# Kernel tuning notes

Hardware: AMD Instinct MI355X
Metric: run time of the kernel (lower is better)

## Reference

```python
import jax, jax.numpy as jnp
import numpy as np

TEMPERATURE = 0.1
EPS = 1e-12  # tf.math.l2_normalize epsilon

BATCH = 512
DIM = 256
QUEUE = 65536


def l2_normalize(x, axis=1):
    sq = jnp.sum(x * x, axis=axis, keepdims=True)
    return x * jax.lax.rsqrt(jnp.maximum(sq, EPS))


def setup_inputs() -> dict:
    key = jax.random.key(0)
    k1, k2, k3 = jax.random.split(key, 3)
    projections_1 = jax.random.normal(k1, (BATCH, DIM), dtype=jnp.float32)
    projections_2 = jax.random.normal(k2, (BATCH, DIM), dtype=jnp.float32)
    feature_queue = l2_normalize(jax.random.normal(k3, (QUEUE, DIM), dtype=jnp.float32), axis=1)
    return {"projections_1": projections_1, "projections_2": projections_2, "feature_queue": feature_queue}


def nearest_neighbour(projections, feature_queue):
    # [B, Q] similarity vs the memory queue, 1-NN retrieval + gather
    support_similarities = jnp.einsum('bd,qd->bq', projections, feature_queue)
    nn_idx = jnp.argmax(support_similarities, axis=1)
    nn_projections = feature_queue[nn_idx]  # [B, D]
    # straight-through: forward value is nn, gradient flows to projections
    return projections + jax.lax.stop_gradient(nn_projections - projections)


def reference(projections_1, projections_2, feature_queue):
    p1 = l2_normalize(projections_1, axis=1)
    p2 = l2_normalize(projections_2, axis=1)

    nn1 = nearest_neighbour(p1, feature_queue)
    nn2 = nearest_neighbour(p2, feature_queue)

    s_1_2_1 = jnp.einsum('bd,cd->bc', nn1, p2) / TEMPERATURE
    s_1_2_2 = jnp.einsum('bd,cd->bc', p2, nn1) / TEMPERATURE
    s_2_1_1 = jnp.einsum('bd,cd->bc', nn2, p1) / TEMPERATURE
    s_2_1_2 = jnp.einsum('bd,cd->bc', p1, nn2) / TEMPERATURE

    logits = jnp.concatenate([s_1_2_1, s_1_2_2, s_2_1_1, s_2_1_2], axis=0)  # [4B, B]
    batch = p1.shape[0]
    labels = jnp.tile(jnp.arange(batch), 4)  # [4B]

    # sparse categorical crossentropy from logits
    logp = jax.nn.log_softmax(logits, axis=-1)
    loss = -logp[jnp.arange(4 * batch), labels]  # [4B]

    # FIFO queue update (normalized projections_1 pushed in front)
    new_queue = jnp.concatenate([p1, feature_queue[:-batch]], axis=0)
    return loss, new_queue
```

## Files before the change

kernel.cpp:

```cpp
#include <hip/hip_runtime.h>
#include <stdint.h>


#define BATCH  512
#define DIM    256
#define QUEUE  65536
#define MROWS  1024
#define NGRP   2048
#define MARGIN 0.01f

typedef short bf16x8 __attribute__((ext_vector_type(8)));
typedef float f32x4  __attribute__((ext_vector_type(4)));

__device__ __forceinline__ unsigned int mono_f32(float f) {
    unsigned int u = __float_as_uint(f);
    return (u & 0x80000000u) ? ~u : (u | 0x80000000u);
}
__device__ __forceinline__ float unmono_f32(unsigned int m) {
    unsigned int u = (m & 0x80000000u) ? (m ^ 0x80000000u) : ~m;
    return __uint_as_float(u);
}
__device__ __forceinline__ unsigned short f2bf(float f) {
    unsigned int u = __float_as_uint(f);
    return (unsigned short)((u + 0x7fffu + ((u >> 16) & 1u)) >> 16);
}

__global__ void k1_norm(const float* __restrict__ p1, const float* __restrict__ p2,
                        float* __restrict__ Pn, float* __restrict__ PnT,
                        unsigned short* __restrict__ PhiF, float* __restrict__ outq,
                        int* __restrict__ npairs, unsigned int* __restrict__ rowmaxU,
                        unsigned long long* __restrict__ rowfinal)
{
    const int r = blockIdx.x;
    const int t = threadIdx.x;
    if (t == 0) {
        rowmaxU[r] = 0u;
        rowfinal[r] = 0ull;
        if (r == 0) *npairs = 0;
    }
    const float* src = (r < BATCH) ? p1 : p2;
    const int row = (r < BATCH) ? r : r - BATCH;
    float4 v = ((const float4*)(src + (size_t)row * DIM))[t];
    float sq = v.x*v.x + v.y*v.y + v.z*v.z + v.w*v.w;
    #pragma unroll
    for (int off = 32; off; off >>= 1) sq += __shfl_xor(sq, off, 64);
    sq = fmaxf(sq, 1e-12f);
    float s = rsqrtf(sq);
    s = s * (1.5f - 0.5f * sq * s * s);
    v.x *= s; v.y *= s; v.z *= s; v.w *= s;
    ((float4*)(Pn + (size_t)r * DIM))[t] = v;
    const int k = t * 4;
    PnT[(size_t)(k + 0) * MROWS + r] = v.x;
    PnT[(size_t)(k + 1) * MROWS + r] = v.y;
    PnT[(size_t)(k + 2) * MROWS + r] = v.z;
    PnT[(size_t)(k + 3) * MROWS + r] = v.w;
    short4 b;
    b.x = (short)f2bf(v.x); b.y = (short)f2bf(v.y);
    b.z = (short)f2bf(v.z); b.w = (short)f2bf(v.w);
    {
        const int c = t >> 1;
        const int idx = ((r >> 4) * 8 + (c >> 2)) * 64 + (c & 3) * 16 + (r & 15);
        *(short4*)((char*)PhiF + (size_t)idx * 16 + (t & 1) * 8) = b;
    }
    if (r < BATCH) ((float4*)(outq + (size_t)r * DIM))[t] = v;
}

__global__ void k0_prep(const float* __restrict__ queue, float* __restrict__ outq,
                        char* __restrict__ Qbf)
{
    const int b = blockIdx.x;
    const int t = threadIdx.x;
    const int n0 = b * 64;
    const f32x4* qsrc = (const f32x4*)(queue + (size_t)n0 * DIM);
    f32x4* qdst = (f32x4*)(outq + (size_t)(n0 + BATCH) * DIM);
    char* tile = Qbf + (size_t)b * 32768;
    #pragma unroll 4
    for (int it = 0; it < 16; ++it) {
        const int L = it * 256 + t;
        const int r = L >> 6, h = L & 63;
        f32x4 v = qsrc[(size_t)r * 64 + h];
        if (n0 + r < QUEUE - BATCH)
            __builtin_nontemporal_store(v, qdst + (size_t)r * 64 + h);
        short4 bb;
        bb.x = (short)f2bf(v.x); bb.y = (short)f2bf(v.y);
        bb.z = (short)f2bf(v.z); bb.w = (short)f2bf(v.w);
        const int c16 = h >> 1, hf = h & 1;
        *(short4*)(tile + r * 512 + ((c16 ^ (r & 31)) << 4) + hf * 8) = bb;
    }
}

__device__ __forceinline__ void k2_stage_async(const char* __restrict__ tile,
                                               char* Bsb, int t)
{
    #pragma unroll
    for (int it = 0; it < 8; ++it) {
        const int L = it * 256 + t;
        __builtin_amdgcn_global_load_lds(
            (const __attribute__((address_space(1))) unsigned int*)(tile + (size_t)L * 16),
            (__attribute__((address_space(3))) unsigned int*)(Bsb + L * 16), 16, 0, 0);
    }
}

__global__ __launch_bounds__(256, 2)
void k2_mfma(const unsigned short* __restrict__ PhiF, const char* __restrict__ Qbf,
             float* __restrict__ cand)
{
    __shared__ __align__(16) char Bs[2][32768];
    const int bid = blockIdx.x;
    const int s = bid >> 8;
    const int c = bid & 255;
    const int t  = threadIdx.x;
    const int w  = t >> 6, lane = t & 63;
    const int lr = lane & 15, q = lane >> 4;
    const int mbase = s * 256 + w * 64;
    const char* chunkbase = Qbf + (size_t)(c * 4) * 32768;

    bf16x8 pfr[4][8];
    {
        const char* Pw = (const char*)PhiF;
        const int mt16b = mbase >> 4;
        #pragma unroll
        for (int mj = 0; mj < 4; ++mj)
            #pragma unroll
            for (int ks = 0; ks < 8; ++ks)
                pfr[mj][ks] = *(const bf16x8*)(Pw + ((size_t)((mt16b + mj) * 8 + ks) * 64 + lane) * 16);
    }

    k2_stage_async(chunkbase, Bs[0], t);
    __syncthreads();

    for (int tl = 0; tl < 4; ++tl) {
        if (tl < 3)
            k2_stage_async(chunkbase + (size_t)(tl + 1) * 32768, Bs[(tl + 1) & 1], t);

        char* Bsb = Bs[tl & 1];
        f32x4 acc[4][4];
        #pragma unroll
        for (int i = 0; i < 4; ++i)
            #pragma unroll
            for (int j = 0; j < 4; ++j) acc[i][j] = (f32x4){0.f, 0.f, 0.f, 0.f};

        #pragma unroll
        for (int ks = 0; ks < 8; ++ks) {
            bf16x8 qf[4];
            #pragma unroll
            for (int ni = 0; ni < 4; ++ni) {
                const int r = ni * 16 + lr;
                const int c16 = ks * 4 + q;
                qf[ni] = *(const bf16x8*)(Bsb + r * 512 + ((c16 ^ (r & 31)) << 4));
            }
            #pragma unroll
            for (int ni = 0; ni < 4; ++ni)
                #pragma unroll
                for (int mj = 0; mj < 4; ++mj)
                    acc[ni][mj] = __builtin_amdgcn_mfma_f32_16x16x32_bf16(qf[ni], pfr[mj][ks], acc[ni][mj], 0, 0, 0);
        }

        #pragma unroll
        for (int mj = 0; mj < 4; ++mj) {
            #pragma unroll
            for (int gl = 0; gl < 2; ++gl) {
                f32x4 va = acc[2 * gl][mj], vb = acc[2 * gl + 1][mj];
                float mx = fmaxf(fmaxf(fmaxf(va[0], va[1]), fmaxf(va[2], va[3])),
                                 fmaxf(fmaxf(vb[0], vb[1]), fmaxf(vb[2], vb[3])));
                mx = fmaxf(mx, __shfl_xor(mx, 16, 64));
                mx = fmaxf(mx, __shfl_xor(mx, 32, 64));
                if (q == 0)
                    cand[(size_t)(c * 8 + tl * 2 + gl) * MROWS + (mbase + mj * 16 + lr)] = mx;
            }
        }
        __syncthreads();
    }
}

__global__ void k2b_rowmax(const float* __restrict__ cand, unsigned int* __restrict__ rowmaxU)
{
    const int t  = threadIdx.x;
    const int ml = t & 63, gs = t >> 6;
    const int mc = blockIdx.x & 15, gc = blockIdx.x >> 4;
    const int m  = mc * 64 + ml;
    const int g0 = gc * 128 + gs * 32;
    float mx = -1e30f;
    #pragma unroll 8
    for (int j = 0; j < 32; ++j)
        mx = fmaxf(mx, cand[(size_t)(g0 + j) * MROWS + m]);
    __shared__ float pm[4][64];
    pm[gs][ml] = mx;
    __syncthreads();
    if (gs == 0) {
        mx = fmaxf(fmaxf(pm[0][ml], pm[1][ml]), fmaxf(pm[2][ml], pm[3][ml]));
        atomicMax(rowmaxU + m, mono_f32(mx));
    }
}

__global__ void k2c_filter(const float* __restrict__ cand, const unsigned int* __restrict__ rowmaxU,
                           unsigned int* __restrict__ pairs, int* __restrict__ npairs)
{
    const int t  = threadIdx.x;
    const int ml = t & 63, gs = t >> 6;
    const int mc = blockIdx.x & 15, gc = blockIdx.x >> 4;
    const int m  = mc * 64 + ml;
    const int g0 = gc * 128 + gs * 32;
    const float thr = unmono_f32(rowmaxU[m]) - MARGIN;
    #pragma unroll 8
    for (int j = 0; j < 32; ++j) {
        if (cand[(size_t)(g0 + j) * MROWS + m] >= thr) {
            int p = atomicAdd(npairs, 1);
            pairs[p] = ((unsigned int)m << 16) | (unsigned int)(g0 + j);
        }
    }
}

__global__ __launch_bounds__(256, 4)
void k2d_rescore(const unsigned int* __restrict__ pairs, const int* __restrict__ npairs,
                 const float* __restrict__ Pn, const float* __restrict__ queue,
                 unsigned long long* __restrict__ rowfinal)
{
    const int t = threadIdx.x, w = t >> 6, lane = t & 63;
    const int n = *npairs;
    const int col_l = lane & 31, half = lane >> 5;
    for (int p = blockIdx.x * 4 + w; p < n; p += gridDim.x * 4) {
        const unsigned int pr = pairs[p];
        const int row = pr >> 16, g = pr & 0xffff;
        const int col = g * 32 + col_l;
        const float4* qp = (const float4*)(queue + (size_t)col * DIM + half * 128);
        const float4* pp = (const float4*)(Pn + (size_t)row * DIM + half * 128);
        float4 sv = {0.f, 0.f, 0.f, 0.f};
        #pragma unroll 8
        for (int j = 0; j < 32; ++j) {
            float4 a = pp[j], b = qp[j];
            sv.x = fmaf(a.x, b.x, sv.x); sv.y = fmaf(a.y, b.y, sv.y);
            sv.z = fmaf(a.z, b.z, sv.z); sv.w = fmaf(a.w, b.w, sv.w);
        }
        float s = (sv.x + sv.y) + (sv.z + sv.w);
        s += __shfl_xor(s, 32, 64);
        unsigned long long best = ((unsigned long long)mono_f32(s) << 32)
                                | (unsigned int)(65535 - col);
        #pragma unroll
        for (int off = 1; off <= 16; off <<= 1) {
            unsigned long long o = __shfl_xor(best, off, 64);
            best = best > o ? best : o;
        }
        if (lane == 0) atomicMax(rowfinal + row, best);
    }
}

__global__ void k3_sim(const unsigned long long* __restrict__ rowfinal,
                       const float* __restrict__ queue,
                       const float* __restrict__ PnT, float* __restrict__ S)
{
    const int b  = blockIdx.x;
    const int rb = (b >> 1) * 8;
    const int ch = b & 1;
    const int tid = threadIdx.x;
    const int which = (rb < BATCH) ? 0 : 1;
    const int colbase = which ? 0 : BATCH;
    const int col = colbase + ch * 256 + tid;
    __shared__ float nnv[8][DIM];
    #pragma unroll
    for (int j = 0; j < 8; ++j) {
        const int idx = 65535 - (int)(rowfinal[rb + j] & 0xFFFFull);
        nnv[j][tid] = queue[(size_t)idx * DIM + tid];
    }
    __syncthreads();
    float acc[8];
    #pragma unroll
    for (int j = 0; j < 8; ++j) acc[j] = 0.f;
    for (int k4 = 0; k4 < 64; ++k4) {
        float4 nv[8];
        #pragma unroll
        for (int j = 0; j < 8; ++j) nv[j] = ((const float4*)nnv[j])[k4];
        #pragma unroll
        for (int kk = 0; kk < 4; ++kk) {
            const int k = k4 * 4 + kk;
            const float v0 = PnT[(size_t)k * MROWS + col];
            #pragma unroll
            for (int j = 0; j < 8; ++j) {
                const float nj = ((const float*)&nv[j])[kk];
                acc[j] = fmaf(nj, v0, acc[j]);
            }
        }
    }
    const int i0 = rb & (BATCH - 1);
    float* Sout = S + (size_t)which * (BATCH * BATCH);
    #pragma unroll
    for (int j = 0; j < 8; ++j)
        Sout[(size_t)(i0 + j) * BATCH + ch * 256 + tid] = acc[j] * 10.0f;
}

__global__ void k4_loss(const float* __restrict__ S, float* __restrict__ loss)
{
    const int r = blockIdx.x;
    const int tid = threadIdx.x;
    const int grp = r >> 9;
    const int i = r & 511;
    const float* M = S + (size_t)(grp >> 1) * (BATCH * BATCH);
    float x0, x1;
    if (!(grp & 1)) { x0 = M[(size_t)i * BATCH + tid];  x1 = M[(size_t)i * BATCH + tid + 256]; }
    else            { x0 = M[(size_t)tid * BATCH + i];  x1 = M[(size_t)(tid + 256) * BATCH + i]; }
    const float diag = M[(size_t)i * BATCH + i];
    float mx = fmaxf(x0, x1);
    #pragma unroll
    for (int off = 1; off < 64; off <<= 1) mx = fmaxf(mx, __shfl_xor(mx, off, 64));
    __shared__ float redm[4], reds[4];
    if ((tid & 63) == 0) redm[tid >> 6] = mx;
    __syncthreads();
    mx = fmaxf(fmaxf(redm[0], redm[1]), fmaxf(redm[2], redm[3]));
    float e = __expf(x0 - mx) + __expf(x1 - mx);
    #pragma unroll
    for (int off = 1; off < 64; off <<= 1) e += __shfl_xor(e, off, 64);
    if ((tid & 63) == 0) reds[tid >> 6] = e;
    __syncthreads();
    if (tid == 0)
        loss[r] = mx + logf(reds[0] + reds[1] + reds[2] + reds[3]) - diag;
}

extern "C" void kernel_launch(void* const* d_in, const int* in_sizes, int n_in,
                              void* d_out, int out_size, void* d_ws, size_t ws_size,
                              hipStream_t stream)
{
    const float* p1    = (const float*)d_in[0];
    const float* p2    = (const float*)d_in[1];
    const float* queue = (const float*)d_in[2];
    float* out  = (float*)d_out;
    float* loss = out;
    float* outq = out + 4 * BATCH;

    char* w = (char*)d_ws;
    float* cand = (float*)w;                               w += (size_t)NGRP * MROWS * 4;
    unsigned long long* rowfinal = (unsigned long long*)w; w += MROWS * 8;
    unsigned int* rowmaxU = (unsigned int*)w;              w += MROWS * 4;
    float* Pn  = (float*)w;                                w += (size_t)MROWS * DIM * 4;
    float* PnT = (float*)w;                                w += (size_t)MROWS * DIM * 4;
    unsigned short* PhiF = (unsigned short*)w;             w += (size_t)MROWS * DIM * 2;
    float* S = (float*)w;                                  w += (size_t)2 * BATCH * BATCH * 4;
    int* npairs = (int*)w;                                 w += 16;
    char* Qbf = w;
    unsigned int* pairs = (unsigned int*)Qbf;

    hipLaunchKernelGGL(k1_norm,     dim3(MROWS), dim3(64),  0, stream, p1, p2, Pn, PnT, PhiF, outq,
                       npairs, rowmaxU, rowfinal);
    hipLaunchKernelGGL(k0_prep,     dim3(QUEUE / 64), dim3(256), 0, stream, queue, outq, Qbf);
    hipLaunchKernelGGL(k2_mfma,     dim3(1024), dim3(256), 0, stream, PhiF, Qbf, cand);
    hipLaunchKernelGGL(k2b_rowmax,  dim3(256),   dim3(256), 0, stream, cand, rowmaxU);
    hipLaunchKernelGGL(k2c_filter,  dim3(256),   dim3(256), 0, stream, cand, rowmaxU, pairs, npairs);
    hipLaunchKernelGGL(k2d_rescore, dim3(512),   dim3(256), 0, stream, pairs, npairs, Pn, queue, rowfinal);
    hipLaunchKernelGGL(k3_sim,      dim3(256),   dim3(256), 0, stream, rowfinal, queue, PnT, S);
    hipLaunchKernelGGL(k4_loss,     dim3(4 * BATCH), dim3(256), 0, stream, S, loss);
}
```

Measured before the change: 245.6 us.

## Fuse row-max into MFMA kernel, widen prep stores, remap block order

The k2b_rowmax kernel is removed. Per-row maxima are now accumulated in registers inside k2_mfma and published with atomicMax at the end, which saves one launch and a full re-read of the candidate buffer. k0_prep now processes 32 rows per block and writes 16-byte bf16x8 stores instead of 8-byte ones. k2_mfma's block-to-(slice,chunk) mapping is remapped so that concurrently running blocks share queue chunks in cache. The cost is more atomics issued from the MFMA kernel.

```diff
diff --git a/kernel.cpp b/kernel.cpp
--- a/kernel.cpp
+++ b/kernel.cpp
@@ -65,27 +65,34 @@
     if (r < BATCH) ((float4*)(outq + (size_t)r * DIM))[t] = v;
 }
 
-__global__ void k0_prep(const float* __restrict__ queue, float* __restrict__ outq,
-                        char* __restrict__ Qbf)
+__global__ __launch_bounds__(256)
+void k0_prep(const float* __restrict__ queue, float* __restrict__ outq,
+             char* __restrict__ Qbf)
 {
     const int b = blockIdx.x;
     const int t = threadIdx.x;
-    const int n0 = b * 64;
+    const int n0 = b * 32;
     const f32x4* qsrc = (const f32x4*)(queue + (size_t)n0 * DIM);
     f32x4* qdst = (f32x4*)(outq + (size_t)(n0 + BATCH) * DIM);
-    char* tile = Qbf + (size_t)b * 32768;
-    #pragma unroll 4
-    for (int it = 0; it < 16; ++it) {
+    char* tile = Qbf + (size_t)(b >> 1) * 32768;
+    #pragma unroll
+    for (int it = 0; it < 4; ++it) {
         const int L = it * 256 + t;
-        const int r = L >> 6, h = L & 63;
-        f32x4 v = qsrc[(size_t)r * 64 + h];
-        if (n0 + r < QUEUE - BATCH)
-            __builtin_nontemporal_store(v, qdst + (size_t)r * 64 + h);
-        short4 bb;
-        bb.x = (short)f2bf(v.x); bb.y = (short)f2bf(v.y);
-        bb.z = (short)f2bf(v.z); bb.w = (short)f2bf(v.w);
-        const int c16 = h >> 1, hf = h & 1;
-        *(short4*)(tile + r * 512 + ((c16 ^ (r & 31)) << 4) + hf * 8) = bb;
+        const int r = L >> 5;
+        const int c16 = L & 31;
+        f32x4 v0 = qsrc[(size_t)r * 64 + c16 * 2];
+        f32x4 v1 = qsrc[(size_t)r * 64 + c16 * 2 + 1];
+        if (n0 + r < QUEUE - BATCH) {
+            __builtin_nontemporal_store(v0, qdst + (size_t)r * 64 + c16 * 2);
+            __builtin_nontemporal_store(v1, qdst + (size_t)r * 64 + c16 * 2 + 1);
+        }
+        bf16x8 bb;
+        bb[0] = (short)f2bf(v0.x); bb[1] = (short)f2bf(v0.y);
+        bb[2] = (short)f2bf(v0.z); bb[3] = (short)f2bf(v0.w);
+        bb[4] = (short)f2bf(v1.x); bb[5] = (short)f2bf(v1.y);
+        bb[6] = (short)f2bf(v1.z); bb[7] = (short)f2bf(v1.w);
+        const int rr = ((b & 1) << 5) + r;
+        *(bf16x8*)(tile + rr * 512 + ((c16 ^ (rr & 31)) << 4)) = bb;
     }
 }
 
@@ -103,12 +110,12 @@
 
 __global__ __launch_bounds__(256, 2)
 void k2_mfma(const unsigned short* __restrict__ PhiF, const char* __restrict__ Qbf,
-             float* __restrict__ cand)
+             float* __restrict__ cand, unsigned int* __restrict__ rowmaxU)
 {
     __shared__ __align__(16) char Bs[2][32768];
     const int bid = blockIdx.x;
-    const int s = bid >> 8;
-    const int c = bid & 255;
+    const int c = (bid >> 5) * 8 + (bid & 7);
+    const int s = (bid >> 3) & 3;
     const int t  = threadIdx.x;
     const int w  = t >> 6, lane = t & 63;
     const int lr = lane & 15, q = lane >> 4;
@@ -128,6 +135,8 @@
 
     k2_stage_async(chunkbase, Bs[0], t);
     __syncthreads();
+
+    float rowmx[4] = {-1e30f, -1e30f, -1e30f, -1e30f};
 
     for (int tl = 0; tl < 4; ++tl) {
         if (tl < 3)
@@ -165,31 +174,18 @@
                                  fmaxf(fmaxf(vb[0], vb[1]), fmaxf(vb[2], vb[3])));
                 mx = fmaxf(mx, __shfl_xor(mx, 16, 64));
                 mx = fmaxf(mx, __shfl_xor(mx, 32, 64));
+                rowmx[mj] = fmaxf(rowmx[mj], mx);
                 if (q == 0)
                     cand[(size_t)(c * 8 + tl * 2 + gl) * MROWS + (mbase + mj * 16 + lr)] = mx;
             }
         }
         __syncthreads();
     }
-}
-
-__global__ void k2b_rowmax(const float* __restrict__ cand, unsigned int* __restrict__ rowmaxU)
-{
-    const int t  = threadIdx.x;
-    const int ml = t & 63, gs = t >> 6;
-    const int mc = blockIdx.x & 15, gc = blockIdx.x >> 4;
-    const int m  = mc * 64 + ml;
-    const int g0 = gc * 128 + gs * 32;
-    float mx = -1e30f;
-    #pragma unroll 8
-    for (int j = 0; j < 32; ++j)
-        mx = fmaxf(mx, cand[(size_t)(g0 + j) * MROWS + m]);
-    __shared__ float pm[4][64];
-    pm[gs][ml] = mx;
-    __syncthreads();
-    if (gs == 0) {
-        mx = fmaxf(fmaxf(pm[0][ml], pm[1][ml]), fmaxf(pm[2][ml], pm[3][ml]));
-        atomicMax(rowmaxU + m, mono_f32(mx));
+
+    if (q == 0) {
+        #pragma unroll
+        for (int mj = 0; mj < 4; ++mj)
+            atomicMax(rowmaxU + mbase + mj * 16 + lr, mono_f32(rowmx[mj]));
     }
 }
 
@@ -340,9 +336,8 @@
 
     hipLaunchKernelGGL(k1_norm,     dim3(MROWS), dim3(64),  0, stream, p1, p2, Pn, PnT, PhiF, outq,
                        npairs, rowmaxU, rowfinal);
-    hipLaunchKernelGGL(k0_prep,     dim3(QUEUE / 64), dim3(256), 0, stream, queue, outq, Qbf);
-    hipLaunchKernelGGL(k2_mfma,     dim3(1024), dim3(256), 0, stream, PhiF, Qbf, cand);
-    hipLaunchKernelGGL(k2b_rowmax,  dim3(256),   dim3(256), 0, stream, cand, rowmaxU);
+    hipLaunchKernelGGL(k0_prep,     dim3(QUEUE / 32), dim3(256), 0, stream, queue, outq, Qbf);
+    hipLaunchKernelGGL(k2_mfma,     dim3(1024), dim3(256), 0, stream, PhiF, Qbf, cand, rowmaxU);
     hipLaunchKernelGGL(k2c_filter,  dim3(256),   dim3(256), 0, stream, cand, rowmaxU, pairs, npairs);
     hipLaunchKernelGGL(k2d_rescore, dim3(512),   dim3(256), 0, stream, pairs, npairs, Pn, queue, rowfinal);
     hipLaunchKernelGGL(k3_sim,      dim3(256),   dim3(256), 0, stream, rowfinal, queue, PnT, S);
```

Result: faster. 240.4 us (-2.1%).
